# Optimization experiments

Measured on AMD Instinct MI355X. Metric: run time of the kernel, lower is better.

The kernel has to match this reference:

```python
import jax, jax.numpy as jnp
import numpy as np

N_HEAD = 16


def setup_inputs() -> dict:
    key = jax.random.key(0)
    k0, k1, k2, k3 = jax.random.split(key, 4)
    b, n, d = 4, 2048, 1024
    scale = d ** -0.5
    return {
        "x": jax.random.normal(k0, (b, n, d), jnp.float32),
        "Wk": jax.random.normal(k1, (d, d), jnp.float32) * scale,
        "Wq": jax.random.normal(k2, (d, d), jnp.float32) * scale,
        "Wv": jax.random.normal(k3, (d, d), jnp.float32) * scale,
    }


def reference(x, Wk, Wq, Wv):
    b, n, d = x.shape
    hd = d // N_HEAD
    # Linear layers: y = x @ W^T (torch nn.Linear convention), no bias.
    keys = (x @ Wk.T).reshape(b, n, N_HEAD, hd).transpose(0, 2, 1, 3)     # (b,h,n,hd)
    queries = (x @ Wq.T).reshape(b, n, N_HEAD, hd).transpose(0, 2, 1, 3)  # (b,h,n,hd)
    values = (x @ Wv.T).reshape(b, n, N_HEAD, hd).transpose(0, 2, 1, 3)   # computed but UNUSED, as in source
    del values
    # Source does: attn_scores = keys @ queries.transpose(-1,-2)
    # i.e. scores[b,h,i,j] = k_i . q_j ; softmax over j (query axis); no 1/sqrt(d) scaling.
    attn_scores = jnp.einsum("bhid,bhjd->bhij", keys, queries)
    weights = jax.nn.softmax(attn_scores, axis=-1)
    # Source does: weight_scores @ keys (keys, NOT values)
    weighted = jnp.einsum("bhij,bhjd->bhid", weights, keys)  # (b,h,n,hd)
    # Source reshapes (b,h,n,hd) directly to (b,n,h*hd) WITHOUT transposing back.
    return weighted.reshape(b, n, N_HEAD * hd)
```

## Files before the change

### kernel.cpp

```cpp
#include <hip/hip_runtime.h>
#include <cstdint>
#include <cstddef>

#define NTOK 2048
#define DMODEL 1024
#define HD 64
#define MROWS 8192

using f16x8  = __attribute__((ext_vector_type(8))) _Float16;
using f16x4  = __attribute__((ext_vector_type(4))) _Float16;
using f32x4  = __attribute__((ext_vector_type(4))) float;
using f32x16 = __attribute__((ext_vector_type(16))) float;
using u16x8  = __attribute__((ext_vector_type(8))) unsigned short;
using u32x4  = __attribute__((ext_vector_type(4))) unsigned int;

#define Z16 {0.f,0.f,0.f,0.f,0.f,0.f,0.f,0.f,0.f,0.f,0.f,0.f,0.f,0.f,0.f,0.f}

__device__ __forceinline__ unsigned pkf16(float a, float b) {
  return __builtin_bit_cast(unsigned, __builtin_amdgcn_cvt_pkrtz(a, b));
}
__device__ __forceinline__ void plswap(unsigned &a, unsigned &b) {
  auto r = __builtin_amdgcn_permlane32_swap(a, b, false, false);
  a = r[0]; b = r[1];
}
__device__ __forceinline__ float fexp2(float x) {
  return __builtin_amdgcn_exp2f(x);
}

__global__ __launch_bounds__(256) void cvt_f32_f16(const float* __restrict__ in,
                                                   _Float16* __restrict__ out,
                                                   int n4, float scale) {
  int idx = blockIdx.x * 256 + threadIdx.x;
  if (idx < n4) {
    float4 v = reinterpret_cast<const float4*>(in)[idx];
    f16x4 o;
    o.x = (_Float16)(v.x * scale); o.y = (_Float16)(v.y * scale);
    o.z = (_Float16)(v.z * scale); o.w = (_Float16)(v.w * scale);
    reinterpret_cast<f16x4*>(out)[idx] = o;
  }
}

__global__ __launch_bounds__(256) void cvt_w(const float* __restrict__ Wk,
                                             const float* __restrict__ Wq,
                                             _Float16* __restrict__ Wkb,
                                             _Float16* __restrict__ Wqb) {
  const int idx = blockIdx.x * 256 + threadIdx.x;
  const float* in = blockIdx.y ? Wq : Wk;
  _Float16* out = blockIdx.y ? Wqb : Wkb;
  const float scale = blockIdx.y ? 1.4426950408889634f : 1.0f;
  float4 v = reinterpret_cast<const float4*>(in)[idx];
  f16x4 o;
  o.x = (_Float16)(v.x * scale); o.y = (_Float16)(v.y * scale);
  o.z = (_Float16)(v.z * scale); o.w = (_Float16)(v.w * scale);
  reinterpret_cast<f16x4*>(out)[idx] = o;
}

#define GLDS16(g, l) __builtin_amdgcn_global_load_lds(                      \
    (const __attribute__((address_space(1))) void*)(g),                     \
    (__attribute__((address_space(3))) void*)(l), 16, 0, 0)

__global__ __launch_bounds__(256) void gemm_f16(
    const _Float16* __restrict__ X,
    const _Float16* __restrict__ Wk,
    const _Float16* __restrict__ Wq,
    _Float16* __restrict__ Kb,
    _Float16* __restrict__ Qb) {
  const _Float16* __restrict__ W = blockIdx.z ? Wq : Wk;
  _Float16* __restrict__ Y = blockIdx.z ? Qb : Kb;

  __shared__ _Float16 As[2][128 * 32];
  __shared__ _Float16 Bs[2][128 * 32];

  const int tid = threadIdx.x;
  const int lane = tid & 63;
  const int w = tid >> 6;
  const int m0 = blockIdx.x * 128;
  const int o0 = blockIdx.y * 128;

  const int srow = w * 32 + (lane >> 2);
  const int scol = (lane & 3) * 8;
  const _Float16* xsrc = X + (size_t)(m0 + srow) * DMODEL + scol;
  const _Float16* wsrc = W + (size_t)(o0 + srow) * DMODEL + scol;

  const int wr = w >> 1, wc = w & 1;
  const int arow = lane & 15, kg = lane >> 4;

  f32x4 zero = {0.f, 0.f, 0.f, 0.f};
  f32x4 acc[4][4];
#pragma unroll
  for (int mi = 0; mi < 4; ++mi)
#pragma unroll
    for (int ni = 0; ni < 4; ++ni) acc[mi][ni] = zero;

  GLDS16(xsrc,               &As[0][(w * 32) * 32]);
  GLDS16(xsrc + 16 * DMODEL, &As[0][(w * 32 + 16) * 32]);
  GLDS16(wsrc,               &Bs[0][(w * 32) * 32]);
  GLDS16(wsrc + 16 * DMODEL, &Bs[0][(w * 32 + 16) * 32]);

  for (int kt = 0; kt < 32; ++kt) {
    __syncthreads();
    if (kt + 1 < 32) {
      const int ko = (kt + 1) * 32;
      const int bn = (kt + 1) & 1;
      GLDS16(xsrc + ko,               &As[bn][(w * 32) * 32]);
      GLDS16(xsrc + ko + 16 * DMODEL, &As[bn][(w * 32 + 16) * 32]);
      GLDS16(wsrc + ko,               &Bs[bn][(w * 32) * 32]);
      GLDS16(wsrc + ko + 16 * DMODEL, &Bs[bn][(w * 32 + 16) * 32]);
    }
    const int buf = kt & 1;
    f16x8 af[4], bfr[4];
#pragma unroll
    for (int mi = 0; mi < 4; ++mi)
      af[mi] = *reinterpret_cast<const f16x8*>(
          &As[buf][(wr * 64 + mi * 16 + arow) * 32 + kg * 8]);
#pragma unroll
    for (int ni = 0; ni < 4; ++ni)
      bfr[ni] = *reinterpret_cast<const f16x8*>(
          &Bs[buf][(wc * 64 + ni * 16 + arow) * 32 + kg * 8]);
#pragma unroll
    for (int mi = 0; mi < 4; ++mi)
#pragma unroll
      for (int ni = 0; ni < 4; ++ni)
        acc[mi][ni] = __builtin_amdgcn_mfma_f32_16x16x32_f16(
            af[mi], bfr[ni], acc[mi][ni], 0, 0, 0);
  }

#pragma unroll
  for (int mi = 0; mi < 4; ++mi) {
#pragma unroll
    for (int ni = 0; ni < 4; ++ni) {
#pragma unroll
      for (int r = 0; r < 4; ++r) {
        const int m = m0 + wr * 64 + mi * 16 + kg * 4 + r;
        const int o = o0 + wc * 64 + ni * 16 + arow;
        Y[(size_t)m * DMODEL + o] = (_Float16)acc[mi][ni][r];
      }
    }
  }
}

__global__ __launch_bounds__(256) void pack_qkt(
    const _Float16* __restrict__ Qb,
    const _Float16* __restrict__ Kb,
    _Float16* __restrict__ Qp,
    _Float16* __restrict__ KTp) {
  const int blk = blockIdx.x;
  const int bh = blk >> 5;
  const int t64 = blk & 31;
  const int b = bh >> 4, h = bh & 15;
  const int tid = threadIdx.x;
  const _Float16* Src = blockIdx.y ? Kb : Qb;

  __shared__ _Float16 t[64][72];
#pragma unroll
  for (int rr = 0; rr < 2; ++rr) {
    const int c = tid + rr * 256;
    const int jr = c >> 3, dcol = (c & 7) * 8;
    *reinterpret_cast<f16x8*>(&t[jr][dcol]) =
        *reinterpret_cast<const f16x8*>(
            &Src[(size_t)(b * NTOK + t64 * 64 + jr) * DMODEL + h * HD + dcol]);
  }
  __syncthreads();
  if (blockIdx.y == 0) {
#pragma unroll
    for (int rr = 0; rr < 2; ++rr) {
      const int cI = tid + rr * 256;
      const int rs = cI >> 8, ks = (cI >> 6) & 3, l = cI & 63;
      f16x8 v = *reinterpret_cast<const f16x8*>(
          &t[rs * 32 + (l & 31)][ks * 16 + (l >> 5) * 8]);
      const size_t ch = ((size_t)(bh * 64 + t64 * 2 + rs) * 4 + ks) * 512 + l * 8;
      *reinterpret_cast<f16x8*>(&Qp[ch]) = v;
    }
  } else {
#pragma unroll
    for (int rr = 0; rr < 2; ++rr) {
      const int cI = tid + rr * 256;
      const int ds = cI >> 8, ks = (cI >> 6) & 3, l = cI & 63;
      const int col = ds * 32 + (l & 31);
      const int row0 = ks * 16 + (l >> 5) * 8;
      f16x8 v;
#pragma unroll
      for (int e = 0; e < 8; ++e) v[e] = t[row0 + e][col];
      const size_t ch = (((size_t)(bh * 32 + t64) * 2 + ds) * 4 + ks) * 512 + l * 8;
      *reinterpret_cast<f16x8*>(&KTp[ch]) = v;
    }
  }
}

__global__ __launch_bounds__(256, 3) void attn_mfma(
    const _Float16* __restrict__ Kb,
    const _Float16* __restrict__ Qp,
    const _Float16* __restrict__ KTp,
    float* __restrict__ out) {
  const int bid = blockIdx.x;
  const int myid = (bid & 7) * 128 + (bid >> 3);
  const int bh = myid >> 4;
  const int itile = myid & 15;
  const int b = bh >> 4, h = bh & 15;
  const int tid = threadIdx.x, lane = tid & 63, w = tid >> 6;
  const int l31 = lane & 31;
  const int hi = lane >> 5;
  const int hi8 = hi * 8;
  const int i0 = itile * 128 + w * 32;

  const _Float16* Kh   = Kb + (size_t)b * NTOK * DMODEL + h * HD;
  const _Float16* qpp  = Qp  + (size_t)bh * 131072 + lane * 8;
  const _Float16* ktpp = KTp + (size_t)bh * 131072 + lane * 8;

  __shared__ float lsl[4][32];
  __shared__ float scl[4][32];

  f16x8 kbf[4];
#pragma unroll
  for (int ks = 0; ks < 4; ++ks)
    kbf[ks] = *reinterpret_cast<const f16x8*>(
        &Kh[(size_t)(i0 + l31) * DMODEL + ks * 16 + hi8]);

  const f32x16 z16v = Z16;
  f32x16 o0 = z16v, o1 = z16v;
  float mreg = -1e30f, ls = 0.f;

  for (int jt = 0; jt < 64; ++jt) {
    f16x8 q[4];
#pragma unroll
    for (int ks = 0; ks < 4; ++ks)
      q[ks] = *reinterpret_cast<const f16x8*>(qpp + ((size_t)jt * 4 + ks) * 512);

    f32x16 s = z16v;
    __builtin_amdgcn_s_setprio(1);
#pragma unroll
    for (int ks = 0; ks < 4; ++ks)
      s = __builtin_amdgcn_mfma_f32_32x32x16_f16(q[ks], kbf[ks], s, 0, 0, 0);
    __builtin_amdgcn_s_setprio(0);

    f16x8 kt0[2], kt1[2];
    {
      const size_t base = ((size_t)(jt >> 1) * 8 + (size_t)(jt & 1) * 2) * 512;
#pragma unroll
      for (int kk = 0; kk < 2; ++kk) {
        kt0[kk] = *reinterpret_cast<const f16x8*>(ktpp + base + (size_t)kk * 512);
        kt1[kk] = *reinterpret_cast<const f16x8*>(ktpp + base + (size_t)(4 + kk) * 512);
      }
    }

    float m0 = fmaxf(s[0], s[4]);
    float m1 = fmaxf(s[1], s[5]);
    float m2 = fmaxf(s[2], s[6]);
    float m3 = fmaxf(s[3], s[7]);
#pragma unroll
    for (int r = 8; r < 16; r += 4) {
      m0 = fmaxf(m0, s[r]);
      m1 = fmaxf(m1, s[r + 1]);
      m2 = fmaxf(m2, s[r + 2]);
      m3 = fmaxf(m3, s[r + 3]);
    }
    float pm = fmaxf(fmaxf(m0, m1), fmaxf(m2, m3));
    pm = fmaxf(pm, __shfl_xor(pm, 32));

    if (!__all(pm <= mreg + 8.0f)) {
      const float mn = fmaxf(mreg, pm);
      const float sc = fexp2(mreg - mn);
      ls *= sc;
      mreg = mn;
      scl[w][l31] = sc;
#pragma unroll
      for (int r = 0; r < 16; ++r) {
        const int il = (r & 3) + 8 * (r >> 2) + 4 * hi;
        const float scr = scl[w][il];
        o0[r] *= scr; o1[r] *= scr;
      }
    }

#pragma unroll
    for (int r = 0; r < 16; ++r) s[r] = fexp2(s[r] - mreg);
    {
      float l0 = (s[0] + s[4]) + (s[8] + s[12]);
      float l1 = (s[1] + s[5]) + (s[9] + s[13]);
      float l2 = (s[2] + s[6]) + (s[10] + s[14]);
      float l3 = (s[3] + s[7]) + (s[11] + s[15]);
      ls += (l0 + l1) + (l2 + l3);
    }

    f16x8 pfr[2];
    {
      unsigned a0 = pkf16(s[0], s[1]),  b0 = pkf16(s[4], s[5]);
      unsigned a1 = pkf16(s[2], s[3]),  b1 = pkf16(s[6], s[7]);
      plswap(a0, b0); plswap(a1, b1);
      u32x4 t; t[0] = a0; t[1] = a1; t[2] = b0; t[3] = b1;
      pfr[0] = __builtin_bit_cast(f16x8, t);
      unsigned a2 = pkf16(s[8], s[9]),   b2 = pkf16(s[12], s[13]);
      unsigned a3 = pkf16(s[10], s[11]), b3 = pkf16(s[14], s[15]);
      plswap(a2, b2); plswap(a3, b3);
      t[0] = a2; t[1] = a3; t[2] = b2; t[3] = b3;
      pfr[1] = __builtin_bit_cast(f16x8, t);
    }

    __builtin_amdgcn_s_setprio(1);
#pragma unroll
    for (int kk = 0; kk < 2; ++kk) {
      o0 = __builtin_amdgcn_mfma_f32_32x32x16_f16(pfr[kk], kt0[kk], o0, 0, 0, 0);
      o1 = __builtin_amdgcn_mfma_f32_32x32x16_f16(pfr[kk], kt1[kk], o1, 0, 0, 0);
    }
    __builtin_amdgcn_s_setprio(0);
  }

  lsl[w][l31] = ls + __shfl_xor(ls, 32);
  __syncthreads();
#pragma unroll
  for (int r = 0; r < 16; ++r) {
    const int il = (r & 3) + 8 * (r >> 2) + 4 * hi;
    const float inv = 1.0f / lsl[w][il];
    const size_t rowb = ((size_t)bh * NTOK + i0 + il) * HD;
    out[rowb + l31]      = o0[r] * inv;
    out[rowb + 32 + l31] = o1[r] * inv;
  }
}

extern "C" void kernel_launch(void* const* d_in, const int* in_sizes, int n_in,
                              void* d_out, int out_size, void* d_ws, size_t ws_size,
                              hipStream_t stream) {
  const float* x  = (const float*)d_in[0];
  const float* Wk = (const float*)d_in[1];
  const float* Wq = (const float*)d_in[2];
  float* out = (float*)d_out;

  _Float16* xb  = (_Float16*)d_ws;
  _Float16* Qp  = xb;
  _Float16* Wkb = xb + (size_t)8388608;
  _Float16* Wqb = Wkb + (size_t)1048576;
  _Float16* Kb  = Wqb + (size_t)1048576;
  _Float16* Qb  = Kb + (size_t)8388608;
  _Float16* KTp = Qb;

  cvt_f32_f16<<<8192, 256, 0, stream>>>(x, xb, 2097152, 1.0f);
  cvt_w<<<dim3(1024, 2), 256, 0, stream>>>(Wk, Wq, Wkb, Wqb);

  dim3 ggrid(MROWS / 128, DMODEL / 128, 2);
  gemm_f16<<<ggrid, 256, 0, stream>>>(xb, Wkb, Wqb, Kb, Qb);

  pack_qkt<<<dim3(2048, 2), 256, 0, stream>>>(Qb, Kb, Qp, KTp);

  attn_mfma<<<1024, 256, 0, stream>>>(Kb, Qp, KTp, out);
}
```

Baseline: 184.4 us.

## Split attention key loop across wave pairs and merge partial softmax in LDS

```diff
diff --git a/kernel.cpp b/kernel.cpp
--- a/kernel.cpp
+++ b/kernel.cpp
@@ -193,22 +193,26 @@
     const _Float16* __restrict__ KTp,
     float* __restrict__ out) {
   const int bid = blockIdx.x;
-  const int myid = (bid & 7) * 128 + (bid >> 3);
-  const int bh = myid >> 4;
-  const int itile = myid & 15;
+  const int myid = (bid & 7) * 256 + (bid >> 3);
+  const int bh = myid >> 5;
+  const int itile = myid & 31;
   const int b = bh >> 4, h = bh & 15;
   const int tid = threadIdx.x, lane = tid & 63, w = tid >> 6;
   const int l31 = lane & 31;
   const int hi = lane >> 5;
   const int hi8 = hi * 8;
-  const int i0 = itile * 128 + w * 32;
+  const int i_sub = w & 1;
+  const int jh = w >> 1;
+  const int i0 = itile * 64 + i_sub * 32;
 
   const _Float16* Kh   = Kb + (size_t)b * NTOK * DMODEL + h * HD;
   const _Float16* qpp  = Qp  + (size_t)bh * 131072 + lane * 8;
   const _Float16* ktpp = KTp + (size_t)bh * 131072 + lane * 8;
 
-  __shared__ float lsl[4][32];
   __shared__ float scl[4][32];
+  __shared__ float mM[2][2][32];
+  __shared__ float lsM[2][2][32];
+  __shared__ float obuf[2][32][64];
 
   f16x8 kbf[4];
 #pragma unroll
@@ -220,7 +224,8 @@
   f32x16 o0 = z16v, o1 = z16v;
   float mreg = -1e30f, ls = 0.f;
 
-  for (int jt = 0; jt < 64; ++jt) {
+  const int jt0 = jh * 32;
+  for (int jt = jt0; jt < jt0 + 32; ++jt) {
     f16x8 q[4];
 #pragma unroll
     for (int ks = 0; ks < 4; ++ks)
@@ -304,15 +309,35 @@
     __builtin_amdgcn_s_setprio(0);
   }
 
-  lsl[w][l31] = ls + __shfl_xor(ls, 32);
+  mM[i_sub][jh][l31]  = mreg;
+  lsM[i_sub][jh][l31] = ls + __shfl_xor(ls, 32);
   __syncthreads();
-#pragma unroll
-  for (int r = 0; r < 16; ++r) {
-    const int il = (r & 3) + 8 * (r >> 2) + 4 * hi;
-    const float inv = 1.0f / lsl[w][il];
-    const size_t rowb = ((size_t)bh * NTOK + i0 + il) * HD;
-    out[rowb + l31]      = o0[r] * inv;
-    out[rowb + 32 + l31] = o1[r] * inv;
+
+  if (jh == 1) {
+#pragma unroll
+    for (int r = 0; r < 16; ++r) {
+      const int il = (r & 3) + 8 * (r >> 2) + 4 * hi;
+      const float mS = fmaxf(mM[i_sub][0][il], mM[i_sub][1][il]);
+      const float f = fexp2(mM[i_sub][1][il] - mS);
+      obuf[i_sub][r][lane]      = o0[r] * f;
+      obuf[i_sub][r + 16][lane] = o1[r] * f;
+    }
+  }
+  __syncthreads();
+  if (jh == 0) {
+#pragma unroll
+    for (int r = 0; r < 16; ++r) {
+      const int il = (r & 3) + 8 * (r >> 2) + 4 * hi;
+      const float mA = mM[i_sub][0][il], mB = mM[i_sub][1][il];
+      const float mS = fmaxf(mA, mB);
+      const float fA = fexp2(mA - mS);
+      const float fB = fexp2(mB - mS);
+      const float lsS = lsM[i_sub][0][il] * fA + lsM[i_sub][1][il] * fB;
+      const float inv = 1.0f / lsS;
+      const size_t rowb = ((size_t)bh * NTOK + i0 + il) * HD;
+      out[rowb + l31]      = (o0[r] * fA + obuf[i_sub][r][lane]) * inv;
+      out[rowb + 32 + l31] = (o1[r] * fA + obuf[i_sub][r + 16][lane]) * inv;
+    }
   }
 }
 
@@ -340,5 +365,5 @@
 
   pack_qkt<<<dim3(2048, 2), 256, 0, stream>>>(Qb, Kb, Qp, KTp);
 
-  attn_mfma<<<1024, 256, 0, stream>>>(Kb, Qp, KTp, out);
-}
+  attn_mfma<<<2048, 256, 0, stream>>>(Kb, Qp, KTp, out);
+}
```

After: 186.1 us. No clear change (+1.0%).
